# Kernel optimization log

Measured on AMD Instinct MI355X. Metric: run time of the kernel, lower is better.

Reference implementation:

```python
import jax, jax.numpy as jnp
import numpy as np

C = 128          # feature_num
INHI_RANGE = C // 8 + 1   # 17, banded channel window width
HALF = INHI_RANGE // 2    # 8


def conv2d(x, w, b=None, pad=0):
    # x: [N,C,H,W], w: [O,I,kh,kw]
    y = jax.lax.conv_general_dilated(
        x, w, window_strides=(1, 1), padding=[(pad, pad), (pad, pad)],
        dimension_numbers=("NCHW", "OIHW", "NCHW"))
    if b is not None:
        y = y + b[None, :, None, None]
    return y


def maxpool(x, k, s, pad):
    # torch MaxPool2d pads with -inf
    return jax.lax.reduce_window(
        x, -jnp.inf, jax.lax.max,
        window_dimensions=(1, 1, k, k), window_strides=(1, 1, s, s),
        padding=[(0, 0), (0, 0), (pad, pad), (pad, pad)])


def lrn(x):
    # Banded cross-channel inhibition: for channel i, sum x^2 over channels
    # j in [i-HALF, i+HALF] (clamped). Original code does this as a dense
    # (128,C,C) bmm; here it is a windowed channel reduction via cumsum.
    # NOTE: the torch code detaches y (x.clone().detach()), so the
    # denominator is a constant w.r.t. autodiff -> stop_gradient.
    x2 = jax.lax.stop_gradient(x) ** 2                      # [N,C,H,W]
    cs = jnp.cumsum(x2, axis=1)
    cs = jnp.concatenate([jnp.zeros_like(cs[:, :1]), cs], axis=1)  # [N,C+1,H,W]
    idx = jnp.arange(C)
    hi = jnp.minimum(idx + HALF + 1, C)
    lo = jnp.maximum(idx - HALF, 0)
    y = cs[:, hi] - cs[:, lo]                               # windowed sum
    y = (y * (0.001 / INHI_RANGE) + 1.0) ** 0.75
    return x / y


def rcl(x, fw, fb, rw, iters=3):
    f = conv2d(x, fw, fb, pad=1)
    r = lrn(jax.nn.relu(f))
    for _ in range(iters):
        r = lrn(jax.nn.relu(f + conv2d(r, rw, None, pad=1)))
    return r


def setup_inputs() -> dict:
    key = jax.random.key(0)
    ks = jax.random.split(key, 20)
    d = {}
    d["x"] = jax.random.normal(ks[0], (128, 3, 64, 64), jnp.float32)
    d["conv1_w"] = jax.random.normal(ks[1], (C, 3, 5, 5), jnp.float32) * 0.05
    d["conv1_b"] = jnp.zeros((C,), jnp.float32)
    d["bn_g"] = jnp.ones((C,), jnp.float32)
    d["bn_b"] = jnp.zeros((C,), jnp.float32)
    for i, n in enumerate(["2", "3", "4", "5"]):
        d[f"f{n}_w"] = jax.random.normal(ks[2 + 3 * i], (C, C, 3, 3), jnp.float32) * 0.02
        d[f"f{n}_b"] = jnp.zeros((C,), jnp.float32)
        d[f"r{n}_w"] = jax.random.normal(ks[3 + 3 * i], (C, C, 3, 3), jnp.float32) * 0.02
    d["mlp_w"] = jax.random.normal(ks[18], (10, C), jnp.float32) * 0.05
    d["mlp_b"] = jnp.zeros((10,), jnp.float32)
    return d


def reference(x, conv1_w, conv1_b, bn_g, bn_b,
              f2_w, f2_b, r2_w, f3_w, f3_b, r3_w,
              f4_w, f4_b, r4_w, f5_w, f5_b, r5_w,
              mlp_w, mlp_b):
    h = conv2d(x, conv1_w, conv1_b, pad=2)                  # [128,C,64,64]
    # BatchNorm2d (training-mode batch statistics, eps=1e-5)
    mean = h.mean(axis=(0, 2, 3), keepdims=True)
    var = h.var(axis=(0, 2, 3), keepdims=True)
    h = (h - mean) * jax.lax.rsqrt(var + 1e-5)
    h = h * bn_g[None, :, None, None] + bn_b[None, :, None, None]
    h = jax.nn.relu(h)
    h = maxpool(h, 3, 2, 1)                                 # 64 -> 32
    h = rcl(h, f2_w, f2_b, r2_w)                            # dropout = identity (eval)
    h = rcl(h, f3_w, f3_b, r3_w)
    h = maxpool(h, 3, 2, 1)                                 # 32 -> 16
    h = rcl(h, f4_w, f4_b, r4_w)
    h = rcl(h, f5_w, f5_b, r5_w)
    h = maxpool(h, 3, 2, 0)                                 # 16 -> 7
    y = h.max(axis=(2, 3))                                  # global max pool [128,C]
    return y @ mlp_w.T + mlp_b
```

## Files before the change

### kernel.cpp

```cpp
#include <hip/hip_runtime.h>


#define CCH 128
constexpr float KAPPA = 0.001f / 17.0f;

typedef __attribute__((ext_vector_type(8))) _Float16 half8;
typedef __attribute__((ext_vector_type(4))) float f32x4;

union U4 { uint4 v; ushort us[8]; _Float16 h[8]; half8 f; };
union U2 { ushort4 u; _Float16 h[4]; };

__global__ __launch_bounds__(256) void zero_stats(float* __restrict__ s) {
    s[threadIdx.x] = 0.f;
}

__global__ __launch_bounds__(256) void wcvt1(const float* __restrict__ wsrc,
                                             _Float16* __restrict__ wdst)
{
    const int idx = blockIdx.x * 256 + threadIdx.x;
    const int kc = idx >> 12;
    const int rem = idx & 4095;
    const int co = rem >> 5;
    const int kk = rem & 31;
    const int k = kc * 32 + kk;
    wdst[idx] = (k < 75) ? (_Float16)wsrc[co * 75 + k] : (_Float16)0.f;
}

__global__ __launch_bounds__(256, 2) void conv1m(
    const float* __restrict__ x, const _Float16* __restrict__ wc1,
    const float* __restrict__ bias, float* __restrict__ stats,
    _Float16* __restrict__ ph, _Float16* __restrict__ pp)
{
    __shared__ _Float16 xst[3 * 8 * 68];
    __shared__ _Float16 bnc[4 * 64 * 128];
    __shared__ float ps[4][128], ps2[4][128];

    const int bid = blockIdx.x;
    const int n = bid & 127;
    const int strip = bid >> 7;
    const int y0 = strip * 4;
    const int tid = threadIdx.x;
    const int w = tid >> 6, l = tid & 63;
    const int l15 = l & 15, lg = l >> 4;

    const float* xn = x + (size_t)n * 3 * 4096;
    for (int i = tid; i < 3 * 8 * 68; i += 256) {
        int ci = i / (8 * 68);
        int rm = i - ci * (8 * 68);
        int r = rm / 68, c = rm - r * 68;
        int gy = y0 - 2 + r, gx = c - 2;
        float v = ((unsigned)gy < 64u && (unsigned)gx < 64u)
                      ? xn[ci * 4096 + gy * 64 + gx] : 0.f;
        xst[i] = (_Float16)v;
    }

    f32x4 acc[8][4];
    #pragma unroll
    for (int cot = 0; cot < 8; ++cot) {
        f32x4 bv = *(const f32x4*)&bias[cot * 16 + lg * 4];
        #pragma unroll
        for (int pt = 0; pt < 4; ++pt) acc[cot][pt] = bv;
    }
    __syncthreads();

    #pragma unroll
    for (int kc = 0; kc < 3; ++kc) {
        int ba[8];
        #pragma unroll
        for (int j = 0; j < 8; ++j) {
            int k = kc * 32 + lg * 8 + j;
            k = k > 74 ? 74 : k;
            int ci = k / 25;
            int r = k - ci * 25;
            int ky = r / 5;
            int kx = r - ky * 5;
            ba[j] = (ci * 8 + w + ky) * 68 + l15 + kx;
        }
        half8 bf[4];
        #pragma unroll
        for (int pt = 0; pt < 4; ++pt) {
            U4 bb;
            #pragma unroll
            for (int j = 0; j < 8; ++j) bb.h[j] = xst[ba[j] + pt * 16];
            bf[pt] = bb.f;
        }
        const _Float16* wk = wc1 + kc * 4096 + l15 * 32 + lg * 8;
        #pragma unroll
        for (int cot = 0; cot < 8; ++cot) {
            half8 av = *(const half8*)&wk[cot * 512];
            #pragma unroll
            for (int pt = 0; pt < 4; ++pt)
                acc[cot][pt] = __builtin_amdgcn_mfma_f32_16x16x32_f16(
                    av, bf[pt], acc[cot][pt], 0, 0, 0);
        }
    }

    #pragma unroll
    for (int cot = 0; cot < 8; ++cot) {
        float s[4] = {0.f, 0.f, 0.f, 0.f}, s2[4] = {0.f, 0.f, 0.f, 0.f};
        #pragma unroll
        for (int pt = 0; pt < 4; ++pt)
            #pragma unroll
            for (int j = 0; j < 4; ++j) {
                float v = acc[cot][pt][j];
                s[j] += v; s2[j] += v * v;
            }
        #pragma unroll
        for (int o = 1; o < 16; o <<= 1)
            #pragma unroll
            for (int j = 0; j < 4; ++j) {
                s[j]  += __shfl_xor(s[j], o, 64);
                s2[j] += __shfl_xor(s2[j], o, 64);
            }
        if (l15 == 0) {
            #pragma unroll
            for (int j = 0; j < 4; ++j) {
                ps[w][cot * 16 + lg * 4 + j] = s[j];
                ps2[w][cot * 16 + lg * 4 + j] = s2[j];
            }
        }
    }

    #pragma unroll
    for (int cot = 0; cot < 8; ++cot)
        #pragma unroll
        for (int pt = 0; pt < 4; ++pt) {
            int c = pt * 16 + l15;
            int colx = (cot * 16 + lg * 4) ^ ((c & 7) * 8);
            U2 pk;
            pk.h[0] = (_Float16)acc[cot][pt][0];
            pk.h[1] = (_Float16)acc[cot][pt][1];
            pk.h[2] = (_Float16)acc[cot][pt][2];
            pk.h[3] = (_Float16)acc[cot][pt][3];
            *(ushort4*)&bnc[(w * 64 + c) * 128 + colx] = pk.u;
        }
    __syncthreads();

    if (tid < 128) {
        float A = ps[0][tid] + ps[1][tid] + ps[2][tid] + ps[3][tid];
        float B = ps2[0][tid] + ps2[1][tid] + ps2[2][tid] + ps2[3][tid];
        atomicAdd(&stats[tid], A);
        atomicAdd(&stats[tid + 128], B);
    }

    constexpr float NEG = -3.0e38f;
    #pragma unroll
    for (int i = 0; i < 6; ++i) {
        int t = tid + i * 256;
        if (t < 1024) {
            int cg = t & 15, ox = (t >> 4) & 31, oysel = t >> 9;
            float m[8];
            #pragma unroll
            for (int j = 0; j < 8; ++j) m[j] = NEG;
            #pragma unroll
            for (int dy = 0; dy < 3; ++dy) {
                int r = 2 * oysel - 1 + dy;
                if (r < 0) continue;
                #pragma unroll
                for (int dx = 0; dx < 3; ++dx) {
                    int c = 2 * ox - 1 + dx;
                    if ((unsigned)c >= 64u) continue;
                    U4 v;
                    v.v = *(const uint4*)&bnc[(r * 64 + c) * 128 + ((cg * 8) ^ ((c & 7) * 8))];
                    #pragma unroll
                    for (int j = 0; j < 8; ++j) m[j] = fmaxf(m[j], (float)v.h[j]);
                }
            }
            U4 o;
            #pragma unroll
            for (int j = 0; j < 8; ++j) o.h[j] = (_Float16)m[j];
            int oy = strip * 2 + oysel;
            *(uint4*)&ph[((size_t)n * 1024 + oy * 32 + ox) * 128 + cg * 8] = o.v;
        } else if (strip < 15) {
            int t2 = t - 1024;
            int cg = t2 & 15, ox = (t2 >> 4) & 31;
            float m[8];
            #pragma unroll
            for (int j = 0; j < 8; ++j) m[j] = NEG;
            #pragma unroll
            for (int dx = 0; dx < 3; ++dx) {
                int c = 2 * ox - 1 + dx;
                if ((unsigned)c >= 64u) continue;
                U4 v;
                v.v = *(const uint4*)&bnc[(3 * 64 + c) * 128 + ((cg * 8) ^ ((c & 7) * 8))];
                #pragma unroll
                for (int j = 0; j < 8; ++j) m[j] = fmaxf(m[j], (float)v.h[j]);
            }
            U4 o;
            #pragma unroll
            for (int j = 0; j < 8; ++j) o.h[j] = (_Float16)m[j];
            *(uint4*)&pp[(((size_t)n * 15 + strip) * 32 + ox) * 128 + cg * 8] = o.v;
        }
    }
}

__global__ __launch_bounds__(256) void pool_fixr(const _Float16* __restrict__ pp,
                                                 _Float16* __restrict__ ph)
{
    const int idx = blockIdx.x * 256 + threadIdx.x;
    const int cg = idx & 15;
    const int ox = (idx >> 4) & 31;
    const int t = idx >> 9;
    const int s = t % 15;
    const int n = t / 15;
    const _Float16* p = pp + (((size_t)n * 15 + s) * 32 + ox) * 128 + cg * 8;
    _Float16* a = ph + ((size_t)n * 1024 + (2 * s + 2) * 32 + ox) * 128 + cg * 8;
    U4 av, bv;
    av.v = *(const uint4*)a;
    bv.v = *(const uint4*)p;
    #pragma unroll
    for (int j = 0; j < 8; ++j)
        if ((float)bv.h[j] > (float)av.h[j]) av.h[j] = bv.h[j];
    *(uint4*)a = av.v;
}

__global__ __launch_bounds__(128) void bn_finalize(
    const float* __restrict__ stats, const float* __restrict__ g,
    const float* __restrict__ b, float* __restrict__ scsh)
{
    const int c = threadIdx.x;
    const float M = 128.f * 4096.f;
    float mean = stats[c] / M;
    float var = stats[c + 128] / M - mean * mean;
    float rstd = rsqrtf(var + 1e-5f);
    float sc = g[c] * rstd;
    scsh[c] = sc;
    scsh[c + 128] = b[c] - mean * sc;
}

__global__ __launch_bounds__(256) void bnrelu(
    const _Float16* __restrict__ ph, const float* __restrict__ scsh,
    _Float16* __restrict__ out)
{
    const int idx = blockIdx.x * 256 + threadIdx.x;
    const int cg = idx & 15;
    const size_t e = (size_t)(idx >> 4) * 128 + cg * 8;
    U4 v; v.v = *(const uint4*)&ph[e];
    U4 o;
    #pragma unroll
    for (int j = 0; j < 8; ++j) {
        int co = cg * 8 + j;
        float f = (float)v.h[j] * scsh[co] + scsh[co + 128];
        o.h[j] = (_Float16)fmaxf(f, 0.f);
    }
    *(uint4*)&out[e] = o.v;
}

__global__ __launch_bounds__(256) void wcvt(const float* __restrict__ wsrc,
                                            _Float16* __restrict__ wdst)
{
    const int idx = blockIdx.x * 256 + threadIdx.x;
    const int t = idx >> 14;
    const int rem = idx & 16383;
    const int co = rem >> 7;
    const int ci = rem & 127;
    wdst[idx] = (_Float16)wsrc[(co * 128 + ci) * 9 + t];
}

template<int H, bool ADD_F>
__global__ __launch_bounds__(256, 1) void conv3f(
    const _Float16* __restrict__ in, const _Float16* __restrict__ wb,
    const float* __restrict__ bias, _Float16* __restrict__ fbuf,
    _Float16* __restrict__ outp)
{
    constexpr int W = H, HW = H * W;
    constexpr int XP = W + 2;
    constexpr int PITCH = 40;
    constexpr int ROWS = 10;
    constexpr int PTN = (H == 32) ? 4 : 2;
    constexpr int NPIX = PTN * 16;
    constexpr int WROW = 40;
    constexpr int WOFF = 9 * 128 * WROW;
    constexpr int STAGE = ROWS * XP * PITCH;
    constexpr int TASKS = ROWS * W * 4;
    constexpr int NIT = (TASKS + 255) / 256;
    constexpr int WNIT = 18;
    constexpr int LOG4W = (H == 32) ? 7 : 6;
    constexpr int LDSH = WOFF + STAGE;

    __shared__ _Float16 xs[LDSH];

    const int bid = blockIdx.x;
    const int slot = bid >> 3;
    const int n = (bid & 7) + 8 * (slot & 15);
    const int y0 = (slot >> 4) * 8;
    const int tid = threadIdx.x;
    const int w = tid >> 6, l = tid & 63;
    const int l15 = l & 15, lg = l >> 4;

    for (int i = tid; i < STAGE / 2; i += 256) ((uint*)(xs + WOFF))[i] = 0;

    f32x4 acc[8][PTN];
    #pragma unroll
    for (int cot = 0; cot < 8; ++cot) {
        f32x4 bv = {0.f, 0.f, 0.f, 0.f};
        if constexpr (!ADD_F) bv = *(const f32x4*)&bias[cot * 16 + lg * 4];
        #pragma unroll
        for (int pt = 0; pt < PTN; ++pt) acc[cot][pt] = bv;
    }

    const _Float16* inb = in + (size_t)n * HW * 128;
    uint4 stg[NIT];
    uint4 wreg[WNIT];

    auto issue = [&](int c0) {
        #pragma unroll
        for (int i = 0; i < NIT; ++i) {
            int t = tid + i * 256;
            uint4 v = {0u, 0u, 0u, 0u};
            if (TASKS % 256 == 0 || t < TASKS) {
                int g = t & 3, xx = (t >> 2) & (W - 1), yl = t >> LOG4W;
                int gy = y0 - 1 + yl;
                if ((unsigned)gy < (unsigned)H)
                    v = *(const uint4*)&inb[((size_t)(gy * W + xx)) * 128 + c0 + g * 8];
            }
            stg[i] = v;
        }
    };
    auto commit = [&]() {
        #pragma unroll
        for (int i = 0; i < NIT; ++i) {
            int t = tid + i * 256;
            if (TASKS % 256 == 0 || t < TASKS) {
                int g = t & 3, xx = (t >> 2) & (W - 1), yl = t >> LOG4W;
                *(uint4*)&xs[WOFF + (yl * XP + xx + 1) * PITCH + g * 8] = stg[i];
            }
        }
    };
    auto wissue = [&](int c0) {
        #pragma unroll
        for (int i = 0; i < WNIT; ++i) {
            int tsk = tid + i * 256;
            int g = tsk & 3, co = (tsk >> 2) & 127, tp = tsk >> 9;
            wreg[i] = *(const uint4*)&wb[tp * 16384 + co * 128 + c0 + g * 8];
        }
    };
    auto wcommit = [&]() {
        #pragma unroll
        for (int i = 0; i < WNIT; ++i) {
            int tsk = tid + i * 256;
            int g = tsk & 3, co = (tsk >> 2) & 127, tp = tsk >> 9;
            *(uint4*)&xs[(tp * 128 + co) * WROW + g * 8] = wreg[i];
        }
    };

    int bofs[PTN];
    #pragma unroll
    for (int pt = 0; pt < PTN; ++pt) {
        int row_l = 2 * w + ((H == 32) ? (pt >> 1) : pt);
        int xb = ((H == 32) ? (pt & 1) * 16 : 0) + l15;
        bofs[pt] = WOFF + ((row_l + 1) * XP + xb + 1) * PITCH + lg * 8;
    }
    const int wlane = l15 * WROW + lg * 8;

    issue(0);
    wissue(0);
    __syncthreads();
    commit();
    wcommit();
    issue(32);
    wissue(32);
    __syncthreads();

    for (int cc = 0; cc < 4; ++cc) {
        #pragma unroll
        for (int ky = -1; ky <= 1; ++ky)
            #pragma unroll
            for (int kx = -1; kx <= 1; ++kx) {
                const int t9 = (ky + 1) * 3 + (kx + 1);
                half8 bf[PTN];
                #pragma unroll
                for (int pt = 0; pt < PTN; ++pt)
                    bf[pt] = *(const half8*)&xs[bofs[pt] + (ky * XP + kx) * PITCH];
                const int wbase = t9 * (128 * WROW) + wlane;
                #pragma unroll
                for (int coh = 0; coh < 2; ++coh) {
                    half8 av[4];
                    #pragma unroll
                    for (int j = 0; j < 4; ++j)
                        av[j] = *(const half8*)&xs[wbase + (coh * 4 + j) * (16 * WROW)];
                    #pragma unroll
                    for (int j = 0; j < 4; ++j)
                        #pragma unroll
                        for (int pt = 0; pt < PTN; ++pt)
                            acc[coh * 4 + j][pt] = __builtin_amdgcn_mfma_f32_16x16x32_f16(
                                av[j], bf[pt], acc[coh * 4 + j][pt], 0, 0, 0);
                }
            }
        if (cc < 3) {
            __syncthreads();
            commit();
            wcommit();
            if (cc < 2) { issue((cc + 2) * 32); wissue((cc + 2) * 32); }
            __syncthreads();
        }
    }

    __syncthreads();
    _Float16* bx = xs + w * (NPIX * 128);
    #pragma unroll
    for (int a = 0; a < 8; ++a)
        #pragma unroll
        for (int pt = 0; pt < PTN; ++pt) {
            const int wpx = pt * 16 + l15;
            const int col = (a * 16 + lg * 4) ^ ((wpx & 7) * 8);
            U2 pk;
            pk.h[0] = (_Float16)acc[a][pt][0];
            pk.h[1] = (_Float16)acc[a][pt][1];
            pk.h[2] = (_Float16)acc[a][pt][2];
            pk.h[3] = (_Float16)acc[a][pt][3];
            *(ushort4*)&bx[wpx * 128 + col] = pk.u;
        }
    __syncthreads();

    if (H == 32 || l < 32) {
        const int px = l & (NPIX - 1);
        const int p3 = px & 7;
        U4 sv[16];
        #pragma unroll
        for (int g = 0; g < 16; ++g)
            sv[g].v = *(const uint4*)&bx[px * 128 + ((g ^ p3) * 8)];

        const int row_l = 2 * w + ((H == 32) ? (px >> 5) : (px >> 4));
        const int xo = px & (W - 1);
        const size_t gbase = ((size_t)n * HW + (size_t)(y0 + row_l) * W + xo) * 128;

        if constexpr (ADD_F) {
            #pragma unroll
            for (int g = 0; g < 16; ++g) {
                U4 fv; fv.v = *(const uint4*)&fbuf[gbase + g * 8];
                #pragma unroll
                for (int j = 0; j < 8; ++j)
                    sv[g].h[j] = (_Float16)((float)sv[g].h[j] + (float)fv.h[j]);
            }
        } else {
            #pragma unroll
            for (int g = 0; g < 16; ++g)
                *(uint4*)&fbuf[gbase + g * 8] = sv[g].v;
        }

        float ring[17], zr[9], wsum = 0.f;
        #pragma unroll
        for (int i = 0; i < 17; ++i) ring[i] = 0.f;
        #pragma unroll
        for (int i = 0; i < 9; ++i) zr[i] = 0.f;
        U4 ob;
        #pragma unroll
        for (int c = 0; c < 136; ++c) {
            float z = 0.f;
            if (c < 128) {
                float v = (float)sv[c >> 3].h[c & 7];
                z = v > 0.f ? v : 0.f;
            }
            float zz = z * z;
            wsum += zz - ring[c % 17];
            ring[c % 17] = zz;
            zr[c % 9] = z;
            if (c >= 8) {
                int o = c - 8;
                float p75 = exp2f(-0.75f * log2f(wsum * KAPPA + 1.f));
                ob.h[o & 7] = (_Float16)(zr[(c + 1) % 9] * p75);
                if ((o & 7) == 7) *(uint4*)&outp[gbase + (o & ~7)] = ob.v;
            }
        }
    }
}

__global__ __launch_bounds__(256) void pool32v(const _Float16* __restrict__ in,
                                               _Float16* __restrict__ out)
{
    const int idx = blockIdx.x * 256 + threadIdx.x;
    const int cg = idx & 15;
    const int opix = (idx >> 4) & 255;
    const int n = idx >> 12;
    const int oy = opix >> 4, ox = opix & 15;
    const _Float16* ib = in + (size_t)n * 1024 * 128 + cg * 8;
    float m[8] = {0.f, 0.f, 0.f, 0.f, 0.f, 0.f, 0.f, 0.f};
    #pragma unroll
    for (int dy = -1; dy <= 1; ++dy) {
        int iy = 2 * oy + dy;
        if ((unsigned)iy >= 32u) continue;
        #pragma unroll
        for (int dx = -1; dx <= 1; ++dx) {
            int ix = 2 * ox + dx;
            if ((unsigned)ix >= 32u) continue;
            U4 v; v.v = *(const uint4*)&ib[(size_t)(iy * 32 + ix) * 128];
            #pragma unroll
            for (int i = 0; i < 8; ++i) m[i] = fmaxf(m[i], (float)v.h[i]);
        }
    }
    U4 o;
    #pragma unroll
    for (int i = 0; i < 8; ++i) o.h[i] = (_Float16)m[i];
    *(uint4*)&out[((size_t)n * 256 + opix) * 128 + cg * 8] = o.v;
}

__global__ __launch_bounds__(256) void gmax2(const _Float16* __restrict__ in,
                                             float* __restrict__ g)
{
    const int idx = blockIdx.x * 256 + threadIdx.x;
    const int c8 = idx & 15;
    const int n = idx >> 4;
    const _Float16* ib = in + (size_t)n * 256 * 128 + c8 * 8;
    float m[8] = {0.f, 0.f, 0.f, 0.f, 0.f, 0.f, 0.f, 0.f};
    for (int y = 0; y < 15; ++y)
        #pragma unroll
        for (int x = 0; x < 15; ++x) {
            U4 v; v.v = *(const uint4*)&ib[(size_t)(y * 16 + x) * 128];
            #pragma unroll
            for (int i = 0; i < 8; ++i) m[i] = fmaxf(m[i], (float)v.h[i]);
        }
    float* gb = g + n * 128 + c8 * 8;
    *(float4*)&gb[0] = {m[0], m[1], m[2], m[3]};
    *(float4*)&gb[4] = {m[4], m[5], m[6], m[7]};
}

__global__ __launch_bounds__(256) void mlp_k(
    const float* __restrict__ g, const float* __restrict__ w,
    const float* __restrict__ b, float* __restrict__ out)
{
    const int idx = blockIdx.x * 256 + threadIdx.x;
    if (idx >= 1280) return;
    const int n = idx / 10, k = idx - n * 10;
    float acc = b[k];
    for (int c = 0; c < CCH; ++c) acc += g[n * CCH + c] * w[k * CCH + c];
    out[idx] = acc;
}

extern "C" void kernel_launch(void* const* d_in, const int* in_sizes, int n_in,
                              void* d_out, int out_size, void* d_ws, size_t ws_size,
                              hipStream_t stream)
{
    const float* x   = (const float*)d_in[0];
    const float* w1  = (const float*)d_in[1];
    const float* b1  = (const float*)d_in[2];
    const float* bng = (const float*)d_in[3];
    const float* bnb = (const float*)d_in[4];
    const float* fw[4] = {(const float*)d_in[5],  (const float*)d_in[8],
                          (const float*)d_in[11], (const float*)d_in[14]};
    const float* fb[4] = {(const float*)d_in[6],  (const float*)d_in[9],
                          (const float*)d_in[12], (const float*)d_in[15]};
    const float* rw[4] = {(const float*)d_in[7],  (const float*)d_in[10],
                          (const float*)d_in[13], (const float*)d_in[16]};
    const float* mw = (const float*)d_in[17];
    const float* mb = (const float*)d_in[18];
    float* out = (float*)d_out;

    _Float16* ws16 = (_Float16*)d_ws;
    _Float16* buf0 = ws16;
    _Float16* buf1 = ws16 + 16777216;
    _Float16* Fb32 = ws16 + 2 * 16777216;
    _Float16* base3 = ws16 + 3 * 16777216;
    _Float16* A16a = base3;
    _Float16* A16b = base3 + 4194304;
    _Float16* F16  = base3 + 2 * 4194304;
    _Float16* Wb   = base3 + 3 * 4194304;
    float* stats = (float*)(Wb + 8 * 147456);
    float* scsh  = stats + 256;
    float* gm    = scsh + 256;
    _Float16* Pp  = (_Float16*)(gm + 16384);
    _Float16* Wc1 = Pp + 7864320;
    _Float16* PH  = buf1;

    zero_stats<<<1, 256, 0, stream>>>(stats);
    wcvt1<<<48, 256, 0, stream>>>(w1, Wc1);
    conv1m<<<2048, 256, 0, stream>>>(x, Wc1, b1, stats, PH, Pp);
    pool_fixr<<<3840, 256, 0, stream>>>(Pp, PH);
    bn_finalize<<<1, 128, 0, stream>>>(stats, bng, bnb, scsh);
    bnrelu<<<8192, 256, 0, stream>>>(PH, scsh, buf0);

    const float* lw[8] = {fw[0], rw[0], fw[1], rw[1], fw[2], rw[2], fw[3], rw[3]};
    for (int i = 0; i < 8; ++i)
        wcvt<<<576, 256, 0, stream>>>(lw[i], Wb + i * 147456);

    _Float16* cur = buf0;
    _Float16* alt = buf1;
    for (int s = 0; s < 2; ++s) {
        conv3f<32, false><<<512, 256, 0, stream>>>(cur, Wb + (2*s) * 147456, fb[s], Fb32, alt);
        { _Float16* t = cur; cur = alt; alt = t; }
        for (int it = 0; it < 3; ++it) {
            conv3f<32, true><<<512, 256, 0, stream>>>(cur, Wb + (2*s+1) * 147456, nullptr, Fb32, alt);
            { _Float16* t = cur; cur = alt; alt = t; }
        }
    }
    pool32v<<<2048, 256, 0, stream>>>(cur, A16a);

    _Float16* cur16 = A16a;
    _Float16* alt16 = A16b;
    for (int s = 2; s < 4; ++s) {
        conv3f<16, false><<<256, 256, 0, stream>>>(cur16, Wb + (2*s) * 147456, fb[s], F16, alt16);
        { _Float16* t = cur16; cur16 = alt16; alt16 = t; }
        for (int it = 0; it < 3; ++it) {
            conv3f<16, true><<<256, 256, 0, stream>>>(cur16, Wb + (2*s+1) * 147456, nullptr, F16, alt16);
            { _Float16* t = cur16; cur16 = alt16; alt16 = t; }
        }
    }
    gmax2<<<8, 256, 0, stream>>>(cur16, gm);
    mlp_k<<<5, 256, 0, stream>>>(gm, mw, mb, out);
}
```

Measured before the change: 1.306 ms.

## Fuse 16x16 RCL stages, pooling and global max into one per-image kernel

```diff
diff --git a/kernel.cpp b/kernel.cpp
--- a/kernel.cpp
+++ b/kernel.cpp
@@ -257,25 +257,25 @@
     wdst[idx] = (_Float16)wsrc[(co * 128 + ci) * 9 + t];
 }
 
-template<int H, bool ADD_F>
+template<bool ADD_F>
 __global__ __launch_bounds__(256, 1) void conv3f(
     const _Float16* __restrict__ in, const _Float16* __restrict__ wb,
     const float* __restrict__ bias, _Float16* __restrict__ fbuf,
     _Float16* __restrict__ outp)
 {
-    constexpr int W = H, HW = H * W;
-    constexpr int XP = W + 2;
+    constexpr int W = 32, HW = 1024;
+    constexpr int XP = 34;
     constexpr int PITCH = 40;
     constexpr int ROWS = 10;
-    constexpr int PTN = (H == 32) ? 4 : 2;
-    constexpr int NPIX = PTN * 16;
+    constexpr int PTN = 4;
+    constexpr int NPIX = 64;
     constexpr int WROW = 40;
     constexpr int WOFF = 9 * 128 * WROW;
     constexpr int STAGE = ROWS * XP * PITCH;
     constexpr int TASKS = ROWS * W * 4;
-    constexpr int NIT = (TASKS + 255) / 256;
+    constexpr int NIT = 5;
     constexpr int WNIT = 18;
-    constexpr int LOG4W = (H == 32) ? 7 : 6;
+    constexpr int LOG4W = 7;
     constexpr int LDSH = WOFF + STAGE;
 
     __shared__ _Float16 xs[LDSH];
@@ -308,10 +308,10 @@
         for (int i = 0; i < NIT; ++i) {
             int t = tid + i * 256;
             uint4 v = {0u, 0u, 0u, 0u};
-            if (TASKS % 256 == 0 || t < TASKS) {
+            {
                 int g = t & 3, xx = (t >> 2) & (W - 1), yl = t >> LOG4W;
                 int gy = y0 - 1 + yl;
-                if ((unsigned)gy < (unsigned)H)
+                if ((unsigned)gy < (unsigned)W)
                     v = *(const uint4*)&inb[((size_t)(gy * W + xx)) * 128 + c0 + g * 8];
             }
             stg[i] = v;
@@ -321,10 +321,8 @@
         #pragma unroll
         for (int i = 0; i < NIT; ++i) {
             int t = tid + i * 256;
-            if (TASKS % 256 == 0 || t < TASKS) {
-                int g = t & 3, xx = (t >> 2) & (W - 1), yl = t >> LOG4W;
-                *(uint4*)&xs[WOFF + (yl * XP + xx + 1) * PITCH + g * 8] = stg[i];
-            }
+            int g = t & 3, xx = (t >> 2) & (W - 1), yl = t >> LOG4W;
+            *(uint4*)&xs[WOFF + (yl * XP + xx + 1) * PITCH + g * 8] = stg[i];
         }
     };
     auto wissue = [&](int c0) {
@@ -347,8 +345,8 @@
     int bofs[PTN];
     #pragma unroll
     for (int pt = 0; pt < PTN; ++pt) {
-        int row_l = 2 * w + ((H == 32) ? (pt >> 1) : pt);
-        int xb = ((H == 32) ? (pt & 1) * 16 : 0) + l15;
+        int row_l = 2 * w + (pt >> 1);
+        int xb = (pt & 1) * 16 + l15;
         bofs[pt] = WOFF + ((row_l + 1) * XP + xb + 1) * PITCH + lg * 8;
     }
     const int wlane = l15 * WROW + lg * 8;
@@ -413,15 +411,15 @@
         }
     __syncthreads();
 
-    if (H == 32 || l < 32) {
-        const int px = l & (NPIX - 1);
+    {
+        const int px = l;
         const int p3 = px & 7;
         U4 sv[16];
         #pragma unroll
         for (int g = 0; g < 16; ++g)
             sv[g].v = *(const uint4*)&bx[px * 128 + ((g ^ p3) * 8)];
 
-        const int row_l = 2 * w + ((H == 32) ? (px >> 5) : (px >> 4));
+        const int row_l = 2 * w + (px >> 5);
         const int xo = px & (W - 1);
         const size_t gbase = ((size_t)n * HW + (size_t)(y0 + row_l) * W + xo) * 128;
 
@@ -466,53 +464,184 @@
     }
 }
 
-__global__ __launch_bounds__(256) void pool32v(const _Float16* __restrict__ in,
-                                               _Float16* __restrict__ out)
-{
-    const int idx = blockIdx.x * 256 + threadIdx.x;
-    const int cg = idx & 15;
-    const int opix = (idx >> 4) & 255;
-    const int n = idx >> 12;
-    const int oy = opix >> 4, ox = opix & 15;
-    const _Float16* ib = in + (size_t)n * 1024 * 128 + cg * 8;
-    float m[8] = {0.f, 0.f, 0.f, 0.f, 0.f, 0.f, 0.f, 0.f};
-    #pragma unroll
-    for (int dy = -1; dy <= 1; ++dy) {
-        int iy = 2 * oy + dy;
-        if ((unsigned)iy >= 32u) continue;
-        #pragma unroll
-        for (int dx = -1; dx <= 1; ++dx) {
-            int ix = 2 * ox + dx;
-            if ((unsigned)ix >= 32u) continue;
-            U4 v; v.v = *(const uint4*)&ib[(size_t)(iy * 32 + ix) * 128];
-            #pragma unroll
-            for (int i = 0; i < 8; ++i) m[i] = fmaxf(m[i], (float)v.h[i]);
-        }
-    }
-    U4 o;
-    #pragma unroll
-    for (int i = 0; i < 8; ++i) o.h[i] = (_Float16)m[i];
-    *(uint4*)&out[((size_t)n * 256 + opix) * 128 + cg * 8] = o.v;
-}
-
-__global__ __launch_bounds__(256) void gmax2(const _Float16* __restrict__ in,
-                                             float* __restrict__ g)
-{
-    const int idx = blockIdx.x * 256 + threadIdx.x;
-    const int c8 = idx & 15;
-    const int n = idx >> 4;
-    const _Float16* ib = in + (size_t)n * 256 * 128 + c8 * 8;
-    float m[8] = {0.f, 0.f, 0.f, 0.f, 0.f, 0.f, 0.f, 0.f};
-    for (int y = 0; y < 15; ++y)
-        #pragma unroll
-        for (int x = 0; x < 15; ++x) {
-            U4 v; v.v = *(const uint4*)&ib[(size_t)(y * 16 + x) * 128];
-            #pragma unroll
-            for (int i = 0; i < 8; ++i) m[i] = fmaxf(m[i], (float)v.h[i]);
-        }
-    float* gb = g + n * 128 + c8 * 8;
-    *(float4*)&gb[0] = {m[0], m[1], m[2], m[3]};
-    *(float4*)&gb[4] = {m[4], m[5], m[6], m[7]};
+__global__ __launch_bounds__(512, 1) void rcl16(
+    const _Float16* __restrict__ a32, const _Float16* __restrict__ wbl,
+    const float* __restrict__ fb4, const float* __restrict__ fb5,
+    float* __restrict__ gm)
+{
+    __shared__ _Float16 Al[256 * 128];
+    __shared__ _Float16 Fl[256 * 128];
+    __shared__ float psm[4][128];
+
+    const int n = blockIdx.x;
+    const int tid = threadIdx.x;
+    const int w = tid >> 6, l = tid & 63;
+    const int l15 = l & 15, lg = l >> 4;
+    const half8 zero8 = {(_Float16)0, (_Float16)0, (_Float16)0, (_Float16)0,
+                         (_Float16)0, (_Float16)0, (_Float16)0, (_Float16)0};
+
+    const _Float16* ib = a32 + (size_t)n * 1024 * 128;
+    #pragma unroll
+    for (int i = 0; i < 8; ++i) {
+        int t = tid + i * 512;
+        int cg = t & 15, opix = t >> 4;
+        int oy = opix >> 4, ox = opix & 15;
+        float m[8] = {0.f, 0.f, 0.f, 0.f, 0.f, 0.f, 0.f, 0.f};
+        #pragma unroll
+        for (int dy = -1; dy <= 1; ++dy) {
+            int iy = 2 * oy + dy;
+            if ((unsigned)iy >= 32u) continue;
+            #pragma unroll
+            for (int dx = -1; dx <= 1; ++dx) {
+                int ix = 2 * ox + dx;
+                if ((unsigned)ix >= 32u) continue;
+                U4 v; v.v = *(const uint4*)&ib[(size_t)(iy * 32 + ix) * 128 + cg * 8];
+                #pragma unroll
+                for (int j = 0; j < 8; ++j) m[j] = fmaxf(m[j], (float)v.h[j]);
+            }
+        }
+        U4 o;
+        #pragma unroll
+        for (int j = 0; j < 8; ++j) o.h[j] = (_Float16)m[j];
+        *(uint4*)&Al[opix * 128 + ((cg * 8) ^ ((opix & 7) * 8))] = o.v;
+    }
+    __syncthreads();
+
+    for (int s = 0; s < 2; ++s) {
+        const float* bias = s ? fb5 : fb4;
+        for (int it = 0; it < 4; ++it) {
+            const _Float16* wlay = wbl + (size_t)(2 * s + (it ? 1 : 0)) * 147456;
+            const _Float16* wl = wlay + l15 * 128 + lg * 8;
+
+            f32x4 acc[8][2];
+            #pragma unroll
+            for (int a = 0; a < 8; ++a) {
+                f32x4 bv = {0.f, 0.f, 0.f, 0.f};
+                if (it == 0) bv = *(const f32x4*)&bias[a * 16 + lg * 4];
+                acc[a][0] = bv; acc[a][1] = bv;
+            }
+
+            for (int c0 = 0; c0 < 128; c0 += 32) {
+                #pragma unroll
+                for (int ky = -1; ky <= 1; ++ky)
+                    #pragma unroll
+                    for (int kx = -1; kx <= 1; ++kx) {
+                        const int t9 = (ky + 1) * 3 + (kx + 1);
+                        half8 bf[2];
+                        #pragma unroll
+                        for (int pt = 0; pt < 2; ++pt) {
+                            int row = 2 * w + pt;
+                            int r2 = row + ky, x2 = l15 + kx;
+                            bool ok = (unsigned)r2 < 16u && (unsigned)x2 < 16u;
+                            int rpx = ok ? (r2 * 16 + x2) : (row * 16 + l15);
+                            half8 v = *(const half8*)&Al[rpx * 128 +
+                                          ((c0 + lg * 8) ^ ((rpx & 7) * 8))];
+                            bf[pt] = ok ? v : zero8;
+                        }
+                        const _Float16* wt = wl + t9 * 16384 + c0;
+                        #pragma unroll
+                        for (int coh = 0; coh < 2; ++coh) {
+                            half8 av[4];
+                            #pragma unroll
+                            for (int j = 0; j < 4; ++j)
+                                av[j] = *(const half8*)&wt[(coh * 4 + j) * 2048];
+                            #pragma unroll
+                            for (int j = 0; j < 4; ++j)
+                                #pragma unroll
+                                for (int pt = 0; pt < 2; ++pt)
+                                    acc[coh * 4 + j][pt] =
+                                        __builtin_amdgcn_mfma_f32_16x16x32_f16(
+                                            av[j], bf[pt], acc[coh * 4 + j][pt], 0, 0, 0);
+                        }
+                    }
+            }
+            __syncthreads();
+
+            #pragma unroll
+            for (int a = 0; a < 8; ++a)
+                #pragma unroll
+                for (int pt = 0; pt < 2; ++pt) {
+                    int px = (2 * w + pt) * 16 + l15;
+                    int col = (a * 16 + lg * 4) ^ ((px & 7) * 8);
+                    U2 pk;
+                    if (it == 0) {
+                        pk.h[0] = (_Float16)acc[a][pt][0];
+                        pk.h[1] = (_Float16)acc[a][pt][1];
+                        pk.h[2] = (_Float16)acc[a][pt][2];
+                        pk.h[3] = (_Float16)acc[a][pt][3];
+                        *(ushort4*)&Fl[px * 128 + col] = pk.u;
+                    } else {
+                        U2 cur; cur.u = *(const ushort4*)&Fl[px * 128 + col];
+                        pk.h[0] = (_Float16)(acc[a][pt][0] + (float)cur.h[0]);
+                        pk.h[1] = (_Float16)(acc[a][pt][1] + (float)cur.h[1]);
+                        pk.h[2] = (_Float16)(acc[a][pt][2] + (float)cur.h[2]);
+                        pk.h[3] = (_Float16)(acc[a][pt][3] + (float)cur.h[3]);
+                    }
+                    *(ushort4*)&Al[px * 128 + col] = pk.u;
+                }
+            __syncthreads();
+
+            {
+                const int px = tid & 255;
+                const int seg = tid >> 8;
+                const int p3 = px & 7;
+                const int cstart = seg ? 56 : 0;
+                const int gb0 = cstart >> 3;
+                const int zlim = 128 - cstart;
+                const int wlo = seg ? 16 : 8;
+                const int whi = wlo + 64;
+
+                U4 sv[10];
+                #pragma unroll
+                for (int i = 0; i < 10; ++i) {
+                    int g = gb0 + i; g = g > 15 ? 15 : g;
+                    sv[i].v = *(const uint4*)&Al[px * 128 + ((g ^ p3) * 8)];
+                }
+                __syncthreads();
+
+                float ring[17], zr[9], wsum = 0.f;
+                #pragma unroll
+                for (int i = 0; i < 17; ++i) ring[i] = 0.f;
+                #pragma unroll
+                for (int i = 0; i < 9; ++i) zr[i] = 0.f;
+                U4 ob;
+                #pragma unroll
+                for (int cl = 0; cl < 80; ++cl) {
+                    float v = (float)sv[cl >> 3].h[cl & 7];
+                    float z = (cl < zlim && v > 0.f) ? v : 0.f;
+                    float zz = z * z;
+                    wsum += zz - ring[cl % 17];
+                    ring[cl % 17] = zz;
+                    zr[cl % 9] = z;
+                    if (cl >= 8) {
+                        const int q = (cl - 8) & 7;
+                        float p75 = exp2f(-0.75f * log2f(wsum * KAPPA + 1.f));
+                        ob.h[q] = (_Float16)(zr[(cl + 1) % 9] * p75);
+                        if (q == 7 && cl >= wlo && cl < whi) {
+                            const int o7 = cstart + cl - 15;
+                            *(uint4*)&Al[px * 128 + (((o7 >> 3) ^ p3) * 8)] = ob.v;
+                        }
+                    }
+                }
+            }
+            __syncthreads();
+        }
+    }
+
+    {
+        int c = tid & 127, q = tid >> 7;
+        float m = 0.f;
+        for (int p = q * 64; p < q * 64 + 64; ++p) {
+            int py = p >> 4, pxx = p & 15;
+            if (py < 15 && pxx < 15)
+                m = fmaxf(m, (float)Al[p * 128 + (c ^ ((p & 7) * 8))]);
+        }
+        psm[q][c] = m;
+        __syncthreads();
+        if (tid < 128)
+            gm[n * 128 + tid] = fmaxf(fmaxf(psm[0][tid], psm[1][tid]),
+                                      fmaxf(psm[2][tid], psm[3][tid]));
+    }
 }
 
 __global__ __launch_bounds__(256) void mlp_k(
@@ -551,9 +680,6 @@
     _Float16* buf1 = ws16 + 16777216;
     _Float16* Fb32 = ws16 + 2 * 16777216;
     _Float16* base3 = ws16 + 3 * 16777216;
-    _Float16* A16a = base3;
-    _Float16* A16b = base3 + 4194304;
-    _Float16* F16  = base3 + 2 * 4194304;
     _Float16* Wb   = base3 + 3 * 4194304;
     float* stats = (float*)(Wb + 8 * 147456);
     float* scsh  = stats + 256;
@@ -576,25 +702,14 @@
     _Float16* cur = buf0;
     _Float16* alt = buf1;
     for (int s = 0; s < 2; ++s) {
-        conv3f<32, false><<<512, 256, 0, stream>>>(cur, Wb + (2*s) * 147456, fb[s], Fb32, alt);
+        conv3f<false><<<512, 256, 0, stream>>>(cur, Wb + (2*s) * 147456, fb[s], Fb32, alt);
         { _Float16* t = cur; cur = alt; alt = t; }
         for (int it = 0; it < 3; ++it) {
-            conv3f<32, true><<<512, 256, 0, stream>>>(cur, Wb + (2*s+1) * 147456, nullptr, Fb32, alt);
+            conv3f<true><<<512, 256, 0, stream>>>(cur, Wb + (2*s+1) * 147456, nullptr, Fb32, alt);
             { _Float16* t = cur; cur = alt; alt = t; }
         }
     }
-    pool32v<<<2048, 256, 0, stream>>>(cur, A16a);
-
-    _Float16* cur16 = A16a;
-    _Float16* alt16 = A16b;
-    for (int s = 2; s < 4; ++s) {
-        conv3f<16, false><<<256, 256, 0, stream>>>(cur16, Wb + (2*s) * 147456, fb[s], F16, alt16);
-        { _Float16* t = cur16; cur16 = alt16; alt16 = t; }
-        for (int it = 0; it < 3; ++it) {
-            conv3f<16, true><<<256, 256, 0, stream>>>(cur16, Wb + (2*s+1) * 147456, nullptr, F16, alt16);
-            { _Float16* t = cur16; cur16 = alt16; alt16 = t; }
-        }
-    }
-    gmax2<<<8, 256, 0, stream>>>(cur16, gm);
+
+    rcl16<<<128, 512, 0, stream>>>(cur, Wb + 4 * 147456, fb[2], fb[3], gm);
     mlp_k<<<5, 256, 0, stream>>>(gm, mw, mb, out);
 }
```

Measured after the change: 1.491 ms. 14.2% more time.
